# Kernel optimization log

Hardware: AMD Instinct MI355X
Metric: run time of the kernel (lower is better)

## Reference

```python
import jax, jax.numpy as jnp
import numpy as np

N_NODES = 50000
N_EDGES = 800000
IN_DIM = 128
HID_DIM = 128
N_CLASSES = 40


def setup_inputs() -> dict:
    key = jax.random.key(0)
    ks = jax.random.split(key, 12)
    s = 0.05
    inp = {
        "X": jax.random.normal(ks[0], (N_NODES, IN_DIM), jnp.float32),
        "A": jax.random.randint(ks[1], (2, N_EDGES), 0, N_NODES, dtype=jnp.int64),
        "W0": jax.random.normal(ks[2], (HID_DIM, IN_DIM), jnp.float32) * s,
        "b0": jnp.zeros((HID_DIM,), jnp.float32),
        "W1": jax.random.normal(ks[3], (HID_DIM, HID_DIM), jnp.float32) * s,
        "b1": jnp.zeros((HID_DIM,), jnp.float32),
        "W2": jax.random.normal(ks[4], (HID_DIM, HID_DIM), jnp.float32) * s,
        "b2": jnp.zeros((HID_DIM,), jnp.float32),
        "W3": jax.random.normal(ks[5], (HID_DIM, HID_DIM), jnp.float32) * s,
        "b3": jnp.zeros((HID_DIM,), jnp.float32),
        "Wf": jax.random.normal(ks[6], (N_CLASSES, HID_DIM), jnp.float32) * s,
        "bf": jnp.zeros((N_CLASSES,), jnp.float32),
    }
    return inp


def _gcn_conv(x, W, b, src, dst):
    # FrobeniusNormGCNConv: normalize weight by Frobenius norm, then standard GCNConv
    Wn = W / jnp.linalg.norm(W)
    h = x @ Wn.T  # [N, out]
    # gcn_norm with self-loops (edge weight 1.0): deg over targets + 1 self loop
    ones = jnp.ones((dst.shape[0],), h.dtype)
    deg = jax.ops.segment_sum(ones, dst, num_segments=N_NODES) + 1.0
    dinv = jax.lax.rsqrt(deg)  # [N]
    norm = dinv[src] * dinv[dst]  # [E]
    # scatter-add of normalized source messages into targets
    agg = jax.ops.segment_sum(norm[:, None] * h[src], dst, num_segments=N_NODES)
    # self-loop contribution: dinv[i]^2 * h[i]; bias added after aggregation
    return agg + (dinv * dinv)[:, None] * h + b


def reference(X, A, W0, b0, W1, b1, W2, b2, W3, b3, Wf, bf):
    src, dst = A[0], A[1]
    h = _gcn_conv(X, W0, b0, src, dst)
    skip = h
    for W, b in ((W1, b1), (W2, b2), (W3, b3)):
        h = _gcn_conv(h, W, b, src, dst)
        h = jax.nn.relu(h)
        h = h + skip  # residual skip (dropout identity in eval mode)
        skip = h
    return h @ Wf.T + bf
```

## Files before the change

kernel.cpp:

```cpp
#include <hip/hip_runtime.h>

#define N_NODES_C 50000
#define N_EDGES_C 800000
#define DIM 128
#define NCLS 40
#define SCAN_NB ((N_NODES_C + 255) / 256)
#define F2B_NB ((N_NODES_C * DIM / 4) / 256)

typedef __attribute__((ext_vector_type(8))) short bf16x8;
typedef __attribute__((ext_vector_type(4))) float f32x4;

__device__ inline float bf2f(unsigned short u) {
    union { unsigned int i; float f; } c;
    c.i = ((unsigned int)u) << 16;
    return c.f;
}
__device__ inline unsigned short f2bf(float f) {
    union { float f; unsigned int i; } c;
    c.f = f;
    unsigned int x = c.i;
    x += 0x7fffu + ((x >> 16) & 1u);
    return (unsigned short)(x >> 16);
}
__device__ inline void add4b(float4& a, const ushort4& u) {
    a.x += bf2f(u.x);
    a.y += bf2f(u.y);
    a.z += bf2f(u.z);
    a.w += bf2f(u.w);
}

__global__ __launch_bounds__(256) void k_pre(const float* __restrict__ X,
                                             const float* __restrict__ W0,
                                             const float* __restrict__ W1,
                                             const float* __restrict__ W2,
                                             const float* __restrict__ W3,
                                             unsigned short* __restrict__ Xb,
                                             unsigned short* __restrict__ Wb,
                                             float* __restrict__ scale_inv) {
    int b = blockIdx.x;
    if (b < F2B_NB) {
        int i = b * 256 + threadIdx.x;
        float4 v = reinterpret_cast<const float4*>(X)[i];
        reinterpret_cast<ushort4*>(Xb)[i] =
            make_ushort4(f2bf(v.x), f2bf(v.y), f2bf(v.z), f2bf(v.w));
        return;
    }
    b -= F2B_NB;
    if (b < 64) {
        int m = b >> 4;
        int idx = (b & 15) * 256 + threadIdx.x;
        const float* W = m == 0 ? W0 : m == 1 ? W1 : m == 2 ? W2 : W3;
        float4 v = reinterpret_cast<const float4*>(W)[idx];
        reinterpret_cast<ushort4*>(Wb + (size_t)m * DIM * DIM)[idx] =
            make_ushort4(f2bf(v.x), f2bf(v.y), f2bf(v.z), f2bf(v.w));
        return;
    }
    b -= 64;
    const float* W = b == 0 ? W0 : b == 1 ? W1 : b == 2 ? W2 : W3;
    float s = 0.f;
    for (int i = threadIdx.x; i < DIM * DIM; i += 256) {
        float v = W[i];
        s += v * v;
    }
    #pragma unroll
    for (int off = 32; off >= 1; off >>= 1) s += __shfl_down(s, off);
    __shared__ float red[4];
    int lane = threadIdx.x & 63, wid = threadIdx.x >> 6;
    if (lane == 0) red[wid] = s;
    __syncthreads();
    if (threadIdx.x == 0) {
        float tot = red[0] + red[1] + red[2] + red[3];
        scale_inv[b] = 1.0f / sqrtf(tot);
    }
}

__global__ void k_deg(const int* __restrict__ A, int* __restrict__ cnt, int E) {
    int e = blockIdx.x * 256 + threadIdx.x;
    if (e >= E) return;
    atomicAdd(&cnt[A[E + e]], 1);
}

__global__ __launch_bounds__(256) void k_scan_part(const int* __restrict__ cnt,
                                                   int* __restrict__ partial,
                                                   float* __restrict__ dinv,
                                                   int* __restrict__ fill, int n) {
    int idx = blockIdx.x * 256 + threadIdx.x;
    int v = (idx < n) ? cnt[idx] : 0;
    if (idx < n) {
        dinv[idx] = rsqrtf((float)v + 1.0f);
        fill[idx] = 0;
    }
    int s = v;
    #pragma unroll
    for (int off = 32; off >= 1; off >>= 1) s += __shfl_down(s, off);
    __shared__ int red[4];
    int lane = threadIdx.x & 63, wid = threadIdx.x >> 6;
    if (lane == 0) red[wid] = s;
    __syncthreads();
    if (threadIdx.x == 0) partial[blockIdx.x] = red[0] + red[1] + red[2] + red[3];
}

__global__ __launch_bounds__(256) void k_scan_final(const int* __restrict__ cnt,
                                                    const int* __restrict__ partial,
                                                    int* __restrict__ ptr, int n, int nb) {
    int tid = threadIdx.x, bid = blockIdx.x;
    int lane = tid & 63, wid = tid >> 6;
    int pv = (tid < nb) ? partial[tid] : 0;
    int vb = (tid < bid) ? pv : 0;
    int s1 = vb, s2 = pv;
    #pragma unroll
    for (int off = 32; off >= 1; off >>= 1) {
        s1 += __shfl_down(s1, off);
        s2 += __shfl_down(s2, off);
    }
    __shared__ int r1[4], r2[4];
    if (lane == 0) { r1[wid] = s1; r2[wid] = s2; }
    __syncthreads();
    __shared__ int sbase, stot;
    if (tid == 0) {
        sbase = r1[0] + r1[1] + r1[2] + r1[3];
        stot  = r2[0] + r2[1] + r2[2] + r2[3];
    }
    __syncthreads();
    int idx = bid * 256 + tid;
    int v = (idx < n) ? cnt[idx] : 0;
    int sc = v;
    #pragma unroll
    for (int off = 1; off < 64; off <<= 1) {
        int t = __shfl_up(sc, off);
        if (lane >= off) sc += t;
    }
    __shared__ int wsum[4], wpre[4];
    if (lane == 63) wsum[wid] = sc;
    __syncthreads();
    if (tid == 0) {
        int acc = 0;
        #pragma unroll
        for (int w = 0; w < 4; ++w) { wpre[w] = acc; acc += wsum[w]; }
    }
    __syncthreads();
    if (idx < n) ptr[idx] = sbase + wpre[wid] + sc - v;
    if (bid == 0 && tid == 0) ptr[n] = stot;
}

__global__ void k_fill(const int* __restrict__ A, const int* __restrict__ ptr,
                       int* __restrict__ fill, unsigned short* __restrict__ esrc, int E) {
    int e = blockIdx.x * 256 + threadIdx.x;
    if (e >= E) return;
    int s = A[e];
    int d = A[E + e];
    int pos = ptr[d] + atomicAdd(&fill[d], 1);
    esrc[pos] = (unsigned short)s;
}

__global__ __launch_bounds__(256) void k_gemm_mfma(const unsigned short* __restrict__ Xb,
                                                   const unsigned short* __restrict__ Wb,
                                                   const float* __restrict__ scale_ptr,
                                                   const float* __restrict__ dinv,
                                                   unsigned short* __restrict__ Gb, int N) {
    int tid = threadIdx.x;
    int w = tid >> 6;
    int l = tid & 63;
    int l15 = l & 15;
    int lg = l >> 4;
    int arow = blockIdx.x * 64 + w * 16 + l15;
    if (arow >= N) arow = N - 1;
    float scale = scale_ptr[0];

    f32x4 acc[8];
    #pragma unroll
    for (int ct = 0; ct < 8; ++ct) acc[ct] = f32x4{0.f, 0.f, 0.f, 0.f};

    #pragma unroll
    for (int kc = 0; kc < 4; ++kc) {
        int ko = kc * 32 + lg * 8;
        bf16x8 a = *reinterpret_cast<const bf16x8*>(&Xb[(size_t)arow * DIM + ko]);
        #pragma unroll
        for (int ct = 0; ct < 8; ++ct) {
            bf16x8 b = *reinterpret_cast<const bf16x8*>(&Wb[(size_t)(ct * 16 + l15) * DIM + ko]);
            acc[ct] = __builtin_amdgcn_mfma_f32_16x16x32_bf16(a, b, acc[ct], 0, 0, 0);
        }
    }
    int outrow0 = blockIdx.x * 64 + w * 16 + lg * 4;
    #pragma unroll
    for (int r = 0; r < 4; ++r) {
        int row = outrow0 + r;
        if (row < N) {
            float dv = dinv[row] * scale;
            #pragma unroll
            for (int ct = 0; ct < 8; ++ct)
                Gb[(size_t)row * DIM + ct * 16 + l15] = f2bf(acc[ct][r] * dv);
        }
    }
}

__global__ __launch_bounds__(256) void k_agg(const unsigned short* __restrict__ Gb,
                                             const float* __restrict__ bias,
                                             const float* __restrict__ dinv,
                                             const int* __restrict__ ptr,
                                             const unsigned short* __restrict__ esrc,
                                             const unsigned short* __restrict__ skipb,
                                             unsigned short* __restrict__ outb,
                                             int relu_res, int N) {
    int n = blockIdx.x * 8 + (threadIdx.x >> 5);
    if (n >= N) return;
    int l = threadIdx.x & 31;
    const ushort4* __restrict__ Gv = reinterpret_cast<const ushort4*>(Gb);
    int beg = ptr[n], end = ptr[n + 1];
    float4 a0 = make_float4(0.f, 0.f, 0.f, 0.f), a1 = a0, a2 = a0, a3 = a0;
    int e = beg;
    for (; e + 8 <= end; e += 8) {
        int s0 = esrc[e + 0], s1 = esrc[e + 1], s2 = esrc[e + 2], s3 = esrc[e + 3];
        int s4 = esrc[e + 4], s5 = esrc[e + 5], s6 = esrc[e + 6], s7 = esrc[e + 7];
        ushort4 g0 = Gv[(size_t)s0 * 32 + l];
        ushort4 g1 = Gv[(size_t)s1 * 32 + l];
        ushort4 g2 = Gv[(size_t)s2 * 32 + l];
        ushort4 g3 = Gv[(size_t)s3 * 32 + l];
        ushort4 g4 = Gv[(size_t)s4 * 32 + l];
        ushort4 g5 = Gv[(size_t)s5 * 32 + l];
        ushort4 g6 = Gv[(size_t)s6 * 32 + l];
        ushort4 g7 = Gv[(size_t)s7 * 32 + l];
        add4b(a0, g0);
        add4b(a1, g1);
        add4b(a2, g2);
        add4b(a3, g3);
        add4b(a0, g4);
        add4b(a1, g5);
        add4b(a2, g6);
        add4b(a3, g7);
    }
    for (; e + 4 <= end; e += 4) {
        int s0 = esrc[e + 0], s1 = esrc[e + 1], s2 = esrc[e + 2], s3 = esrc[e + 3];
        ushort4 g0 = Gv[(size_t)s0 * 32 + l];
        ushort4 g1 = Gv[(size_t)s1 * 32 + l];
        ushort4 g2 = Gv[(size_t)s2 * 32 + l];
        ushort4 g3 = Gv[(size_t)s3 * 32 + l];
        add4b(a0, g0);
        add4b(a1, g1);
        add4b(a2, g2);
        add4b(a3, g3);
    }
    for (; e < end; ++e) {
        ushort4 g = Gv[(size_t)esrc[e] * 32 + l];
        add4b(a0, g);
    }
    float4 acc;
    acc.x = (a0.x + a1.x) + (a2.x + a3.x);
    acc.y = (a0.y + a1.y) + (a2.y + a3.y);
    acc.z = (a0.z + a1.z) + (a2.z + a3.z);
    acc.w = (a0.w + a1.w) + (a2.w + a3.w);

    float di = dinv[n];
    ushort4 gu = Gv[(size_t)n * 32 + l];
    float4 b4 = reinterpret_cast<const float4*>(bias)[l];
    float4 v;
    v.x = fmaf(di, acc.x + bf2f(gu.x), b4.x);
    v.y = fmaf(di, acc.y + bf2f(gu.y), b4.y);
    v.z = fmaf(di, acc.z + bf2f(gu.z), b4.z);
    v.w = fmaf(di, acc.w + bf2f(gu.w), b4.w);
    if (relu_res) {
        ushort4 su = reinterpret_cast<const ushort4*>(skipb)[(size_t)n * 32 + l];
        v.x = fmaxf(v.x, 0.f) + bf2f(su.x);
        v.y = fmaxf(v.y, 0.f) + bf2f(su.y);
        v.z = fmaxf(v.z, 0.f) + bf2f(su.z);
        v.w = fmaxf(v.w, 0.f) + bf2f(su.w);
    }
    reinterpret_cast<ushort4*>(outb)[(size_t)n * 32 + l] =
        make_ushort4(f2bf(v.x), f2bf(v.y), f2bf(v.z), f2bf(v.w));
}

__global__ __launch_bounds__(256) void k_final(const unsigned short* __restrict__ Hb,
                                               const float* __restrict__ Wf,
                                               const float* __restrict__ bf,
                                               float* __restrict__ out, int N) {
    __shared__ float Xs[16][68];
    __shared__ float Ws[16][64];
    int tid = threadIdx.x;
    int n0 = blockIdx.x * 64;
    int tx = tid & 15;
    int ty = tid >> 4;
    float acc[4][4] = {};
    for (int k0 = 0; k0 < DIM; k0 += 16) {
        {
            int j = tid >> 2, kq = tid & 3;
            int row = n0 + j;
            if (row >= N) row = N - 1;
            ushort4 x4 = *reinterpret_cast<const ushort4*>(&Hb[(size_t)row * DIM + k0 + kq * 4]);
            Xs[kq * 4 + 0][j] = bf2f(x4.x);
            Xs[kq * 4 + 1][j] = bf2f(x4.y);
            Xs[kq * 4 + 2][j] = bf2f(x4.z);
            Xs[kq * 4 + 3][j] = bf2f(x4.w);
        }
        {
            int o = tid >> 2, kq = tid & 3;
            int om = o < NCLS ? o : o - NCLS;
            const float4 w4 = *reinterpret_cast<const float4*>(&Wf[(size_t)om * DIM + k0 + kq * 4]);
            Ws[kq * 4 + 0][o] = w4.x;
            Ws[kq * 4 + 1][o] = w4.y;
            Ws[kq * 4 + 2][o] = w4.z;
            Ws[kq * 4 + 3][o] = w4.w;
        }
        __syncthreads();
        #pragma unroll
        for (int k = 0; k < 16; ++k) {
            float4 w = *reinterpret_cast<const float4*>(&Ws[k][tx * 4]);
            float4 x = *reinterpret_cast<const float4*>(&Xs[k][ty * 4]);
            float xv[4] = {x.x, x.y, x.z, x.w};
            #pragma unroll
            for (int i = 0; i < 4; ++i) {
                acc[i][0] = fmaf(xv[i], w.x, acc[i][0]);
                acc[i][1] = fmaf(xv[i], w.y, acc[i][1]);
                acc[i][2] = fmaf(xv[i], w.z, acc[i][2]);
                acc[i][3] = fmaf(xv[i], w.w, acc[i][3]);
            }
        }
        __syncthreads();
    }
    if (tx >= 10) return;
    float4 b4 = make_float4(bf[tx * 4], bf[tx * 4 + 1], bf[tx * 4 + 2], bf[tx * 4 + 3]);
    #pragma unroll
    for (int i = 0; i < 4; ++i) {
        int row = n0 + ty * 4 + i;
        if (row < N) {
            float* op = &out[(size_t)row * NCLS + tx * 4];
            op[0] = acc[i][0] + b4.x;
            op[1] = acc[i][1] + b4.y;
            op[2] = acc[i][2] + b4.z;
            op[3] = acc[i][3] + b4.w;
        }
    }
}

extern "C" void kernel_launch(void* const* d_in, const int* in_sizes, int n_in,
                              void* d_out, int out_size, void* d_ws, size_t ws_size,
                              hipStream_t stream) {
    (void)in_sizes; (void)n_in; (void)out_size; (void)ws_size;
    const float* X  = (const float*)d_in[0];
    const int*   A  = (const int*)d_in[1];
    const float* W0 = (const float*)d_in[2];
    const float* b0 = (const float*)d_in[3];
    const float* W1 = (const float*)d_in[4];
    const float* b1 = (const float*)d_in[5];
    const float* W2 = (const float*)d_in[6];
    const float* b2 = (const float*)d_in[7];
    const float* W3 = (const float*)d_in[8];
    const float* b3 = (const float*)d_in[9];
    const float* Wf = (const float*)d_in[10];
    const float* bf = (const float*)d_in[11];
    float* out = (float*)d_out;

    char* base_ws = (char*)d_ws;
    size_t off = 0;
    auto alloc = [&](size_t bytes) -> char* {
        char* p = base_ws + off;
        off = (off + bytes + 255) & ~(size_t)255;
        return p;
    };
    float* scale_inv = (float*)alloc(4 * sizeof(float));
    int*   deg   = (int*)alloc(N_NODES_C * sizeof(int));
    int*   fill  = (int*)alloc(N_NODES_C * sizeof(int));
    int*   ptr   = (int*)alloc((N_NODES_C + 1) * sizeof(int));
    float* dinv  = (float*)alloc(N_NODES_C * sizeof(float));
    int*   part  = (int*)alloc(SCAN_NB * sizeof(int));
    unsigned short* esrc = (unsigned short*)alloc((size_t)N_EDGES_C * sizeof(unsigned short));
    unsigned short* Gb  = (unsigned short*)alloc((size_t)N_NODES_C * DIM * sizeof(unsigned short));
    unsigned short* Xb  = (unsigned short*)alloc((size_t)N_NODES_C * DIM * sizeof(unsigned short));
    unsigned short* Hb1 = (unsigned short*)alloc((size_t)N_NODES_C * DIM * sizeof(unsigned short));
    unsigned short* Hb2 = (unsigned short*)alloc((size_t)N_NODES_C * DIM * sizeof(unsigned short));
    unsigned short* Wb  = (unsigned short*)alloc((size_t)4 * DIM * DIM * sizeof(unsigned short));

    hipMemsetAsync(deg, 0, N_NODES_C * sizeof(int), stream);

    k_pre<<<F2B_NB + 64 + 4, 256, 0, stream>>>(X, W0, W1, W2, W3, Xb, Wb, scale_inv);
    k_deg<<<(N_EDGES_C + 255) / 256, 256, 0, stream>>>(A, deg, N_EDGES_C);
    k_scan_part<<<SCAN_NB, 256, 0, stream>>>(deg, part, dinv, fill, N_NODES_C);
    k_scan_final<<<SCAN_NB, 256, 0, stream>>>(deg, part, ptr, N_NODES_C, SCAN_NB);
    k_fill<<<(N_EDGES_C + 255) / 256, 256, 0, stream>>>(A, ptr, fill, esrc, N_EDGES_C);

    const int gemm_grid = (N_NODES_C + 63) / 64;
    const int agg_grid  = (N_NODES_C + 7) / 8;

    k_gemm_mfma<<<gemm_grid, 256, 0, stream>>>(Xb, Wb + 0 * DIM * DIM, scale_inv + 0, dinv, Gb, N_NODES_C);
    k_agg<<<agg_grid, 256, 0, stream>>>(Gb, b0, dinv, ptr, esrc, nullptr, Hb1, 0, N_NODES_C);
    k_gemm_mfma<<<gemm_grid, 256, 0, stream>>>(Hb1, Wb + 1 * DIM * DIM, scale_inv + 1, dinv, Gb, N_NODES_C);
    k_agg<<<agg_grid, 256, 0, stream>>>(Gb, b1, dinv, ptr, esrc, Hb1, Hb2, 1, N_NODES_C);
    k_gemm_mfma<<<gemm_grid, 256, 0, stream>>>(Hb2, Wb + 2 * DIM * DIM, scale_inv + 2, dinv, Gb, N_NODES_C);
    k_agg<<<agg_grid, 256, 0, stream>>>(Gb, b2, dinv, ptr, esrc, Hb2, Hb1, 1, N_NODES_C);
    k_gemm_mfma<<<gemm_grid, 256, 0, stream>>>(Hb1, Wb + 3 * DIM * DIM, scale_inv + 3, dinv, Gb, N_NODES_C);
    k_agg<<<agg_grid, 256, 0, stream>>>(Gb, b3, dinv, ptr, esrc, Hb1, Hb2, 1, N_NODES_C);
    k_final<<<(N_NODES_C + 63) / 64, 256, 0, stream>>>(Hb2, Wf, bf, out, N_NODES_C);
}
```

Before: 348.7 us.

## Bucket edges by destination for CSR build and widen aggregation loads

Edges are first partitioned into 32 destination-range buckets using shared-memory counters. Degrees are then counted per bucket in LDS, and the CSR fill walks the bucketed edges so that global atomics and scatter writes stay localized. The aggregation kernel now gives each node a full wavefront with four 16-lane groups, each loading 16-byte bf16 vectors for different edges, and combines the groups with cross-lane shuffles. Bucket capacity is fixed at 32768, so a skewed destination distribution would silently drop edges. Only a quarter of lanes do the epilogue, and the packed (d<<16|s) encoding assumes node ids fit in 16 bits, which 50000 does.

New measurement: 353.9 us. Within noise of the previous version (+1.5%).

```diff
diff --git a/kernel.cpp b/kernel.cpp
--- a/kernel.cpp
+++ b/kernel.cpp
@@ -6,6 +6,8 @@
 #define NCLS 40
 #define SCAN_NB ((N_NODES_C + 255) / 256)
 #define F2B_NB ((N_NODES_C * DIM / 4) / 256)
+#define NBUK 32
+#define BCAP 32768
 
 typedef __attribute__((ext_vector_type(8))) short bf16x8;
 typedef __attribute__((ext_vector_type(4))) float f32x4;
@@ -22,11 +24,11 @@
     x += 0x7fffu + ((x >> 16) & 1u);
     return (unsigned short)(x >> 16);
 }
-__device__ inline void add4b(float4& a, const ushort4& u) {
-    a.x += bf2f(u.x);
-    a.y += bf2f(u.y);
-    a.z += bf2f(u.z);
-    a.w += bf2f(u.w);
+__device__ inline void unp8(const uint4& g, float* f) {
+    f[0] = __uint_as_float(g.x << 16); f[1] = __uint_as_float(g.x & 0xFFFF0000u);
+    f[2] = __uint_as_float(g.y << 16); f[3] = __uint_as_float(g.y & 0xFFFF0000u);
+    f[4] = __uint_as_float(g.z << 16); f[5] = __uint_as_float(g.z & 0xFFFF0000u);
+    f[6] = __uint_as_float(g.w << 16); f[7] = __uint_as_float(g.w & 0xFFFF0000u);
 }
 
 __global__ __launch_bounds__(256) void k_pre(const float* __restrict__ X,
@@ -74,10 +76,60 @@
     }
 }
 
-__global__ void k_deg(const int* __restrict__ A, int* __restrict__ cnt, int E) {
-    int e = blockIdx.x * 256 + threadIdx.x;
-    if (e >= E) return;
-    atomicAdd(&cnt[A[E + e]], 1);
+__global__ __launch_bounds__(256) void k_bucket(const int* __restrict__ A,
+                                                int* __restrict__ gcount,
+                                                unsigned int* __restrict__ ebuk, int E) {
+    __shared__ int cnt[NBUK];
+    __shared__ int gbase[NBUK];
+    int tid = threadIdx.x;
+    if (tid < NBUK) cnt[tid] = 0;
+    __syncthreads();
+    int e0 = blockIdx.x * 1024;
+    int s[4], d[4], b[4], r[4];
+    #pragma unroll
+    for (int j = 0; j < 4; ++j) {
+        int e = e0 + j * 256 + tid;
+        if (e < E) {
+            s[j] = A[e];
+            d[j] = A[E + e];
+            b[j] = (int)(((unsigned long long)(unsigned)d[j] * NBUK) / N_NODES_C);
+            r[j] = atomicAdd(&cnt[b[j]], 1);
+        } else {
+            b[j] = -1;
+        }
+    }
+    __syncthreads();
+    if (tid < NBUK) gbase[tid] = atomicAdd(&gcount[tid], cnt[tid]);
+    __syncthreads();
+    #pragma unroll
+    for (int j = 0; j < 4; ++j) {
+        if (b[j] >= 0) {
+            int pos = gbase[b[j]] + r[j];
+            if (pos < BCAP)
+                ebuk[(size_t)b[j] * BCAP + pos] =
+                    ((unsigned)d[j] << 16) | (unsigned)s[j];
+        }
+    }
+}
+
+__global__ __launch_bounds__(256) void k_degb(const unsigned int* __restrict__ ebuk,
+                                              const int* __restrict__ gcount,
+                                              int* __restrict__ deg) {
+    int k = blockIdx.x;
+    int base = (k * N_NODES_C + NBUK - 1) / NBUK;
+    int next = ((k + 1) * N_NODES_C + NBUK - 1) / NBUK;
+    int sz = next - base;
+    __shared__ int dl[1568];
+    for (int i = threadIdx.x; i < sz; i += 256) dl[i] = 0;
+    __syncthreads();
+    int count = gcount[k];
+    if (count > BCAP) count = BCAP;
+    for (int i = threadIdx.x; i < count; i += 256) {
+        int d = (int)(ebuk[(size_t)k * BCAP + i] >> 16);
+        atomicAdd(&dl[d - base], 1);
+    }
+    __syncthreads();
+    for (int i = threadIdx.x; i < sz; i += 256) deg[base + i] = dl[i];
 }
 
 __global__ __launch_bounds__(256) void k_scan_part(const int* __restrict__ cnt,
@@ -143,14 +195,28 @@
     if (bid == 0 && tid == 0) ptr[n] = stot;
 }
 
-__global__ void k_fill(const int* __restrict__ A, const int* __restrict__ ptr,
-                       int* __restrict__ fill, unsigned short* __restrict__ esrc, int E) {
-    int e = blockIdx.x * 256 + threadIdx.x;
-    if (e >= E) return;
-    int s = A[e];
-    int d = A[E + e];
-    int pos = ptr[d] + atomicAdd(&fill[d], 1);
-    esrc[pos] = (unsigned short)s;
+__global__ __launch_bounds__(256) void k_fillb(const unsigned int* __restrict__ ebuk,
+                                               const int* __restrict__ gcount,
+                                               const int* __restrict__ ptr,
+                                               int* __restrict__ fill,
+                                               unsigned short* __restrict__ esrc) {
+    int k = blockIdx.x & (NBUK - 1);
+    int c = blockIdx.x / NBUK;
+    int count = gcount[k];
+    if (count > BCAP) count = BCAP;
+    int i0 = c * 1024;
+    if (i0 >= count) return;
+    #pragma unroll
+    for (int j = 0; j < 4; ++j) {
+        int i = i0 + j * 256 + threadIdx.x;
+        if (i < count) {
+            unsigned v = ebuk[(size_t)k * BCAP + i];
+            int d = (int)(v >> 16);
+            int s = (int)(v & 0xFFFFu);
+            int pos = ptr[d] + atomicAdd(&fill[d], 1);
+            esrc[pos] = (unsigned short)s;
+        }
+    }
 }
 
 __global__ __launch_bounds__(256) void k_gemm_mfma(const unsigned short* __restrict__ Xb,
@@ -202,71 +268,72 @@
                                              const unsigned short* __restrict__ skipb,
                                              unsigned short* __restrict__ outb,
                                              int relu_res, int N) {
-    int n = blockIdx.x * 8 + (threadIdx.x >> 5);
+    int n = blockIdx.x * 4 + (threadIdx.x >> 6);
     if (n >= N) return;
-    int l = threadIdx.x & 31;
-    const ushort4* __restrict__ Gv = reinterpret_cast<const ushort4*>(Gb);
+    int l = threadIdx.x & 63;
+    int grp = l >> 4, li = l & 15;
+    const uint4* __restrict__ Gv = reinterpret_cast<const uint4*>(Gb);
     int beg = ptr[n], end = ptr[n + 1];
-    float4 a0 = make_float4(0.f, 0.f, 0.f, 0.f), a1 = a0, a2 = a0, a3 = a0;
+    float acc[8] = {};
+    float t[8];
     int e = beg;
     for (; e + 8 <= end; e += 8) {
-        int s0 = esrc[e + 0], s1 = esrc[e + 1], s2 = esrc[e + 2], s3 = esrc[e + 3];
-        int s4 = esrc[e + 4], s5 = esrc[e + 5], s6 = esrc[e + 6], s7 = esrc[e + 7];
-        ushort4 g0 = Gv[(size_t)s0 * 32 + l];
-        ushort4 g1 = Gv[(size_t)s1 * 32 + l];
-        ushort4 g2 = Gv[(size_t)s2 * 32 + l];
-        ushort4 g3 = Gv[(size_t)s3 * 32 + l];
-        ushort4 g4 = Gv[(size_t)s4 * 32 + l];
-        ushort4 g5 = Gv[(size_t)s5 * 32 + l];
-        ushort4 g6 = Gv[(size_t)s6 * 32 + l];
-        ushort4 g7 = Gv[(size_t)s7 * 32 + l];
-        add4b(a0, g0);
-        add4b(a1, g1);
-        add4b(a2, g2);
-        add4b(a3, g3);
-        add4b(a0, g4);
-        add4b(a1, g5);
-        add4b(a2, g6);
-        add4b(a3, g7);
+        int s0 = esrc[e + grp];
+        int s1 = esrc[e + 4 + grp];
+        uint4 g0 = Gv[(size_t)s0 * 16 + li];
+        uint4 g1 = Gv[(size_t)s1 * 16 + li];
+        unp8(g0, t);
+        #pragma unroll
+        for (int j = 0; j < 8; ++j) acc[j] += t[j];
+        unp8(g1, t);
+        #pragma unroll
+        for (int j = 0; j < 8; ++j) acc[j] += t[j];
     }
     for (; e + 4 <= end; e += 4) {
-        int s0 = esrc[e + 0], s1 = esrc[e + 1], s2 = esrc[e + 2], s3 = esrc[e + 3];
-        ushort4 g0 = Gv[(size_t)s0 * 32 + l];
-        ushort4 g1 = Gv[(size_t)s1 * 32 + l];
-        ushort4 g2 = Gv[(size_t)s2 * 32 + l];
-        ushort4 g3 = Gv[(size_t)s3 * 32 + l];
-        add4b(a0, g0);
-        add4b(a1, g1);
-        add4b(a2, g2);
-        add4b(a3, g3);
-    }
-    for (; e < end; ++e) {
-        ushort4 g = Gv[(size_t)esrc[e] * 32 + l];
-        add4b(a0, g);
-    }
-    float4 acc;
-    acc.x = (a0.x + a1.x) + (a2.x + a3.x);
-    acc.y = (a0.y + a1.y) + (a2.y + a3.y);
-    acc.z = (a0.z + a1.z) + (a2.z + a3.z);
-    acc.w = (a0.w + a1.w) + (a2.w + a3.w);
-
-    float di = dinv[n];
-    ushort4 gu = Gv[(size_t)n * 32 + l];
-    float4 b4 = reinterpret_cast<const float4*>(bias)[l];
-    float4 v;
-    v.x = fmaf(di, acc.x + bf2f(gu.x), b4.x);
-    v.y = fmaf(di, acc.y + bf2f(gu.y), b4.y);
-    v.z = fmaf(di, acc.z + bf2f(gu.z), b4.z);
-    v.w = fmaf(di, acc.w + bf2f(gu.w), b4.w);
-    if (relu_res) {
-        ushort4 su = reinterpret_cast<const ushort4*>(skipb)[(size_t)n * 32 + l];
-        v.x = fmaxf(v.x, 0.f) + bf2f(su.x);
-        v.y = fmaxf(v.y, 0.f) + bf2f(su.y);
-        v.z = fmaxf(v.z, 0.f) + bf2f(su.z);
-        v.w = fmaxf(v.w, 0.f) + bf2f(su.w);
-    }
-    reinterpret_cast<ushort4*>(outb)[(size_t)n * 32 + l] =
-        make_ushort4(f2bf(v.x), f2bf(v.y), f2bf(v.z), f2bf(v.w));
+        int s0 = esrc[e + grp];
+        uint4 g0 = Gv[(size_t)s0 * 16 + li];
+        unp8(g0, t);
+        #pragma unroll
+        for (int j = 0; j < 8; ++j) acc[j] += t[j];
+    }
+    int rem = end - e;
+    if (grp < rem) {
+        int s0 = esrc[e + grp];
+        uint4 g0 = Gv[(size_t)s0 * 16 + li];
+        unp8(g0, t);
+        #pragma unroll
+        for (int j = 0; j < 8; ++j) acc[j] += t[j];
+    }
+    #pragma unroll
+    for (int j = 0; j < 8; ++j) {
+        acc[j] += __shfl_xor(acc[j], 16);
+        acc[j] += __shfl_xor(acc[j], 32);
+    }
+    if (grp == 0) {
+        float di = dinv[n];
+        uint4 gu = Gv[(size_t)n * 16 + li];
+        float gs[8];
+        unp8(gu, gs);
+        const float4* b4 = reinterpret_cast<const float4*>(bias);
+        float4 ba = b4[li * 2], bb = b4[li * 2 + 1];
+        float bv[8] = {ba.x, ba.y, ba.z, ba.w, bb.x, bb.y, bb.z, bb.w};
+        float v[8];
+        #pragma unroll
+        for (int j = 0; j < 8; ++j) v[j] = fmaf(di, acc[j] + gs[j], bv[j]);
+        if (relu_res) {
+            uint4 su = reinterpret_cast<const uint4*>(skipb)[(size_t)n * 16 + li];
+            float ss[8];
+            unp8(su, ss);
+            #pragma unroll
+            for (int j = 0; j < 8; ++j) v[j] = fmaxf(v[j], 0.f) + ss[j];
+        }
+        uint4 o;
+        o.x = (unsigned)f2bf(v[0]) | ((unsigned)f2bf(v[1]) << 16);
+        o.y = (unsigned)f2bf(v[2]) | ((unsigned)f2bf(v[3]) << 16);
+        o.z = (unsigned)f2bf(v[4]) | ((unsigned)f2bf(v[5]) << 16);
+        o.w = (unsigned)f2bf(v[6]) | ((unsigned)f2bf(v[7]) << 16);
+        reinterpret_cast<uint4*>(outb)[(size_t)n * 16 + li] = o;
+    }
 }
 
 __global__ __launch_bounds__(256) void k_final(const unsigned short* __restrict__ Hb,
@@ -357,11 +424,13 @@
         return p;
     };
     float* scale_inv = (float*)alloc(4 * sizeof(float));
-    int*   deg   = (int*)alloc(N_NODES_C * sizeof(int));
-    int*   fill  = (int*)alloc(N_NODES_C * sizeof(int));
-    int*   ptr   = (int*)alloc((N_NODES_C + 1) * sizeof(int));
-    float* dinv  = (float*)alloc(N_NODES_C * sizeof(float));
-    int*   part  = (int*)alloc(SCAN_NB * sizeof(int));
+    int*   deg    = (int*)alloc(N_NODES_C * sizeof(int));
+    int*   fill   = (int*)alloc(N_NODES_C * sizeof(int));
+    int*   ptr    = (int*)alloc((N_NODES_C + 1) * sizeof(int));
+    float* dinv   = (float*)alloc(N_NODES_C * sizeof(float));
+    int*   part   = (int*)alloc(SCAN_NB * sizeof(int));
+    int*   gcount = (int*)alloc(NBUK * sizeof(int));
+    unsigned int*   ebuk = (unsigned int*)alloc((size_t)NBUK * BCAP * sizeof(unsigned int));
     unsigned short* esrc = (unsigned short*)alloc((size_t)N_EDGES_C * sizeof(unsigned short));
     unsigned short* Gb  = (unsigned short*)alloc((size_t)N_NODES_C * DIM * sizeof(unsigned short));
     unsigned short* Xb  = (unsigned short*)alloc((size_t)N_NODES_C * DIM * sizeof(unsigned short));
@@ -369,16 +438,17 @@
     unsigned short* Hb2 = (unsigned short*)alloc((size_t)N_NODES_C * DIM * sizeof(unsigned short));
     unsigned short* Wb  = (unsigned short*)alloc((size_t)4 * DIM * DIM * sizeof(unsigned short));
 
-    hipMemsetAsync(deg, 0, N_NODES_C * sizeof(int), stream);
+    hipMemsetAsync(gcount, 0, NBUK * sizeof(int), stream);
 
     k_pre<<<F2B_NB + 64 + 4, 256, 0, stream>>>(X, W0, W1, W2, W3, Xb, Wb, scale_inv);
-    k_deg<<<(N_EDGES_C + 255) / 256, 256, 0, stream>>>(A, deg, N_EDGES_C);
+    k_bucket<<<(N_EDGES_C + 1023) / 1024, 256, 0, stream>>>(A, gcount, ebuk, N_EDGES_C);
+    k_degb<<<NBUK, 256, 0, stream>>>(ebuk, gcount, deg);
     k_scan_part<<<SCAN_NB, 256, 0, stream>>>(deg, part, dinv, fill, N_NODES_C);
     k_scan_final<<<SCAN_NB, 256, 0, stream>>>(deg, part, ptr, N_NODES_C, SCAN_NB);
-    k_fill<<<(N_EDGES_C + 255) / 256, 256, 0, stream>>>(A, ptr, fill, esrc, N_EDGES_C);
+    k_fillb<<<NBUK * (BCAP / 1024), 256, 0, stream>>>(ebuk, gcount, ptr, fill, esrc);
 
     const int gemm_grid = (N_NODES_C + 63) / 64;
-    const int agg_grid  = (N_NODES_C + 7) / 8;
+    const int agg_grid  = (N_NODES_C + 3) / 4;
 
     k_gemm_mfma<<<gemm_grid, 256, 0, stream>>>(Xb, Wb + 0 * DIM * DIM, scale_inv + 0, dinv, Gb, N_NODES_C);
     k_agg<<<agg_grid, 256, 0, stream>>>(Gb, b0, dinv, ptr, esrc, nullptr, Hb1, 0, N_NODES_C);
```
